# Performance work log

Hardware: AMD Instinct MI355X
Metric: run time of the kernel (lower is better)

The kernel has to match this reference:

```python
import jax, jax.numpy as jnp
import numpy as np

NH, DQK, DV = 8, 256, 64
B, TI, TO, H, W = 8, 16, 16, 32, 32


def setup_inputs() -> dict:
    key = jax.random.key(0)
    ks = jax.random.split(key, 10)
    def wn(k, shape, fan_in):
        return jax.random.normal(k, shape, jnp.float32) * (1.0 / np.sqrt(fan_in)).astype(np.float32)
    return {
        "v": jax.random.normal(ks[0], (B, TI, DV, H, W), jnp.float32),
        "k": jax.random.normal(ks[1], (B, TI, DQK), jnp.float32),
        "q": jax.random.normal(ks[2], (B, TO, DQK), jnp.float32),
        "prod_mask": jax.random.randint(ks[3], (B, TO, TI), 0, 2, jnp.int32),
        "Wq": wn(ks[4], (DQK, NH * DQK), DQK),   # q_layer: Linear(d_qk, nh*d_qk)
        "bq": jnp.zeros((NH * DQK,), jnp.float32),
        "Wk": wn(ks[5], (DQK, NH * DQK), DQK),   # k_layer
        "bk": jnp.zeros((NH * DQK,), jnp.float32),
        "Wv": wn(ks[6], (NH * DV, DV, 3, 3), DV * 9),  # v_layer: Conv2d(d_v, nh*d_v, 3, pad=1), OIHW
        "bv": jnp.zeros((NH * DV,), jnp.float32),
        "Wp": wn(ks[7], (DV, NH * DV, 1, 1), NH * DV),  # proj_concat: Conv2d(nh*d_v, d_v, 1)
        "bp": jnp.zeros((DV,), jnp.float32),
    }


def _conv(x, w, b, pad):
    y = jax.lax.conv_general_dilated(
        x, w, window_strides=(1, 1), padding=[(pad, pad), (pad, pad)],
        dimension_numbers=("NCHW", "OIHW", "NCHW"))
    return y + b[None, :, None, None]


def reference(v, k, q, prod_mask, Wq, bq, Wk, bk, Wv, bv, Wp, bp):
    Bv, Ti, dv, Hh, Ww = v.shape
    To = q.shape[1]
    # linear projections, split into heads (chunk along feature dim == contiguous blocks)
    pq = (q @ Wq + bq).reshape(Bv, To, NH, DQK)
    pk = (k @ Wk + bk).reshape(Bv, Ti, NH, DQK)
    # 3x3 conv projection of values over all B*T_i frames
    pv = _conv(v.reshape(Bv * Ti, dv, Hh, Ww), Wv, bv, 1).reshape(Bv, Ti, NH, dv, Hh, Ww)
    # scaled dot-product attention, all heads at once
    scores = jnp.einsum("bohd,bihd->bhoi", pq, pk) / jnp.sqrt(jnp.float32(DQK))
    scores = jnp.where(prod_mask[:, None, :, :] == 0, jnp.float32(-1e10), scores)
    weights = jax.nn.softmax(scores, axis=-1)  # softmax over T_i
    pv_flat = pv.reshape(Bv, Ti, NH, dv * Hh * Ww)
    att = jnp.einsum("bhoi,bihf->bohf", weights, pv_flat)  # [B,To,NH,dv*H*W]
    # concat heads along channel dim, then 1x1 conv projection
    concat = att.reshape(Bv * To, NH * dv, Hh, Ww)
    out = _conv(concat, Wp, bp, 0)
    return out.reshape(Bv, To, dv, Hh, Ww)
```

## Files before the change

kernel.cpp:

```cpp
#include <hip/hip_runtime.h>
#include <hip/hip_fp16.h>

#define NH_   8
#define DQK_  256
#define DV_   64
#define NB_   8
#define TI_   16
#define TO_   16
#define HH_   32
#define WW_   32
#define FR_   (NB_*TI_)
#define PX_   (HH_*WW_)

typedef _Float16 f16x8 __attribute__((ext_vector_type(8)));
typedef _Float16 f16x4 __attribute__((ext_vector_type(4)));
typedef float    f32x4 __attribute__((ext_vector_type(4)));

__global__ __launch_bounds__(256) void k_prep(const float* __restrict__ v,
                                              _Float16* __restrict__ v16t) {
    int blk = blockIdx.x;
    int f = blk >> 2;
    int px = ((blk & 3) << 8) + threadIdx.x;
    const float* src = v + (size_t)f * DV_ * PX_;
    _Float16* dst = v16t + (size_t)f * PX_ * DV_ + (size_t)px * DV_;
    f16x8 buf[8];
    #pragma unroll
    for (int cg = 0; cg < 8; ++cg) {
        #pragma unroll
        for (int j = 0; j < 8; ++j)
            buf[cg][j] = (_Float16)src[(cg * 8 + j) * PX_ + px];
    }
    #pragma unroll
    for (int cg = 0; cg < 8; ++cg)
        *(f16x8*)(dst + cg * 8) = buf[cg];
}

__global__ void k_proj(const float* __restrict__ q, const float* __restrict__ kk,
                       const float* __restrict__ Wq, const float* __restrict__ bq,
                       const float* __restrict__ Wk, const float* __restrict__ bk,
                       float* __restrict__ pq, float* __restrict__ pk) {
    __shared__ float qs[32][256];
    int mat = blockIdx.z;
    const float* X  = mat ? kk : q;
    const float* Wm = mat ? Wk : Wq;
    const float* bm = mat ? bk : bq;
    float* out = mat ? pk : pq;
    int t = threadIdx.x;
    int by = blockIdx.y;
    for (int idx = t; idx < 32 * 256; idx += 256) {
        int r = idx >> 8, k2 = idx & 255;
        qs[r][k2] = X[(by * 32 + r) * 256 + k2];
    }
    __syncthreads();
    int nd = blockIdx.x * 64 + (t & 63);
    int jb = (t >> 6) * 8;
    float a[8];
    #pragma unroll
    for (int j = 0; j < 8; ++j) a[j] = 0.f;
    for (int k2 = 0; k2 < 256; ++k2) {
        float wv = Wm[k2 * 2048 + nd];
        #pragma unroll
        for (int j = 0; j < 8; ++j) a[j] += qs[jb + j][k2] * wv;
    }
    float bb = bm[nd];
    #pragma unroll
    for (int j = 0; j < 8; ++j)
        out[(size_t)(by * 32 + jb + j) * 2048 + nd] = a[j] + bb;
}

__global__ void k_scores(const float* __restrict__ pq, const float* __restrict__ pk,
                         const int* __restrict__ mask, float* __restrict__ wsm) {
    __shared__ float lq[16][256];
    __shared__ float lk[16][257];
    int b = blockIdx.x >> 3, n = blockIdx.x & 7;
    int t = threadIdx.x;
    for (int idx = t; idx < 4096; idx += 256) {
        int r = idx >> 8, dd = idx & 255;
        lq[r][dd] = pq[(size_t)(b * 16 + r) * 2048 + n * 256 + dd];
        lk[r][dd] = pk[(size_t)(b * 16 + r) * 2048 + n * 256 + dd];
    }
    __syncthreads();
    int o = t >> 4, i = t & 15;
    float s = 0.f;
    for (int dd = 0; dd < 256; ++dd) s += lq[o][dd] * lk[i][dd];
    s *= 0.0625f;
    if (mask[(b * 16 + o) * 16 + i] == 0) s = -1e10f;
    float mx = s;
    #pragma unroll
    for (int off = 1; off < 16; off <<= 1) mx = fmaxf(mx, __shfl_xor(mx, off, 16));
    float e = __expf(s - mx);
    float sum = e;
    #pragma unroll
    for (int off = 1; off < 16; off <<= 1) sum += __shfl_xor(sum, off, 16);
    wsm[((size_t)(b * 8 + n) * 16 + o) * 16 + i] = e / sum;
}

__global__ void k_fold(const float* __restrict__ Wp, const float* __restrict__ Wv,
                       _Float16* __restrict__ Wf2) {
    int gid = blockIdx.x * 256 + threadIdx.x;
    int l = gid & 63;
    int oct16 = (gid >> 6) & 31;
    int cg = (gid >> 11) & 1;
    int r = gid >> 12;
    int oc = oct16 * 16 + (l & 15);
    int n = oc >> 6, d = oc & 63;
    int cbase = cg * 32 + (l >> 4) * 8;
    float acc[8];
    #pragma unroll
    for (int j = 0; j < 8; ++j) acc[j] = 0.f;
    for (int c2 = 0; c2 < 64; ++c2) {
        float wp = Wp[d * 512 + n * 64 + c2];
        #pragma unroll
        for (int j = 0; j < 8; ++j)
            acc[j] += wp * Wv[((n * 64 + c2) * 64 + cbase + j) * 9 + r];
    }
    #pragma unroll
    for (int j = 0; j < 8; ++j) Wf2[(size_t)gid * 8 + j] = (_Float16)acc[j];
}

__global__ void k_foldbias(const float* __restrict__ Wp, const float* __restrict__ bv,
                           const float* __restrict__ bp, float* __restrict__ bias_out) {
    int d = threadIdx.x;
    float acc = bp[d];
    for (int oc = 0; oc < 512; ++oc) acc += Wp[d * 512 + oc] * bv[oc];
    bias_out[d] = acc;
}

__global__ __launch_bounds__(256) void k_conv(const _Float16* __restrict__ v16t,
                                              const _Float16* __restrict__ Wf2,
                                              _Float16* __restrict__ g) {
    __shared__ _Float16 slab[204 * 64];
    int f = blockIdx.z, mblk = blockIdx.y, pxblk = blockIdx.x;
    int t = threadIdx.x;
    int l = t & 63, wm = t >> 6;

    const _Float16* vb = v16t + (size_t)f * PX_ * DV_;
    for (int task = t; task < 204 * 8; task += 256) {
        int pos = task >> 3, sl = task & 7;
        int yy = pos / 34;
        int xx = pos - yy * 34;
        int y = pxblk * 4 + yy - 1;
        int x = xx - 1;
        uint4 val = make_uint4(0u, 0u, 0u, 0u);
        if ((unsigned)y < 32u && (unsigned)x < 32u)
            val = *(const uint4*)(vb + (y * 32 + x) * 64 + sl * 8);
        int off = pos * 128 + ((sl ^ (pos & 7)) << 4);
        *(uint4*)((char*)slab + off) = val;
    }
    __syncthreads();

    int m = l & 15, kg = l >> 4;
    int pos0[8];
    #pragma unroll
    for (int nt = 0; nt < 8; ++nt) {
        int pxl = nt * 16 + m;
        pos0[nt] = (pxl >> 5) * 34 + (pxl & 31);
    }

    const f16x8* Wf8 = (const f16x8*)Wf2;
    f32x4 acc[2][8];
    #pragma unroll
    for (int mt = 0; mt < 2; ++mt)
        #pragma unroll
        for (int nt = 0; nt < 8; ++nt)
            acc[mt][nt] = (f32x4){0.f, 0.f, 0.f, 0.f};

    #pragma unroll
    for (int cg = 0; cg < 2; ++cg) {
        int slotb = (cg * 4 + kg) << 4;
        #pragma unroll
        for (int r = 0; r < 9; ++r) {
            int dd = (r / 3) * 34 + (r % 3);
            int abase = (r * 2 + cg) * 32 + mblk * 8 + wm * 2;
            f16x8 af0 = Wf8[(size_t)(abase + 0) * 64 + l];
            f16x8 af1 = Wf8[(size_t)(abase + 1) * 64 + l];
            f16x8 bf[8];
            #pragma unroll
            for (int nt = 0; nt < 8; ++nt) {
                int pos = pos0[nt] + dd;
                int off = pos * 128 + (slotb ^ ((pos & 7) << 4));
                bf[nt] = *(const f16x8*)((const char*)slab + off);
            }
            #pragma unroll
            for (int nt = 0; nt < 8; ++nt) {
                acc[0][nt] = __builtin_amdgcn_mfma_f32_16x16x32_f16(af0, bf[nt], acc[0][nt], 0, 0, 0);
                acc[1][nt] = __builtin_amdgcn_mfma_f32_16x16x32_f16(af1, bf[nt], acc[1][nt], 0, 0, 0);
            }
        }
    }

    _Float16* gb = g + (size_t)f * 512 * 1024 + (size_t)pxblk * 128;
    #pragma unroll
    for (int mt = 0; mt < 2; ++mt) {
        int ocbase = (mblk * 8 + wm * 2 + mt) * 16 + kg * 4;
        #pragma unroll
        for (int nt = 0; nt < 8; ++nt) {
            int px = nt * 16 + m;
            #pragma unroll
            for (int e = 0; e < 4; ++e)
                gb[(size_t)(ocbase + e) * 1024 + px] = (_Float16)acc[mt][nt][e];
        }
    }
}

__global__ void k_comb(const _Float16* __restrict__ g, const float* __restrict__ wsm,
                       const float* __restrict__ bias_out, float* __restrict__ out) {
    __shared__ float wl[2048];
    int d = blockIdx.y, b = blockIdx.z;
    int t = threadIdx.x;
    for (int idx = t; idx < 2048; idx += 256) wl[idx] = wsm[(size_t)b * 2048 + idx];
    __syncthreads();
    int px0 = t * 4;
    float acc[16][4];
    #pragma unroll
    for (int o = 0; o < 16; ++o)
        #pragma unroll
        for (int e = 0; e < 4; ++e) acc[o][e] = 0.f;

    for (int i = 0; i < 16; ++i) {
        #pragma unroll
        for (int n = 0; n < 8; ++n) {
            const _Float16* gp = g + ((size_t)((b * 16 + i) * 512 + n * 64 + d)) * 1024 + px0;
            f16x4 hv = *(const f16x4*)gp;
            float g0 = (float)hv[0], g1 = (float)hv[1], g2 = (float)hv[2], g3 = (float)hv[3];
            #pragma unroll
            for (int o = 0; o < 16; ++o) {
                float wv = wl[n * 256 + o * 16 + i];
                acc[o][0] += wv * g0;
                acc[o][1] += wv * g1;
                acc[o][2] += wv * g2;
                acc[o][3] += wv * g3;
            }
        }
    }
    float bo = bias_out[d];
    #pragma unroll
    for (int o = 0; o < 16; ++o) {
        float4 res = make_float4(acc[o][0] + bo, acc[o][1] + bo, acc[o][2] + bo, acc[o][3] + bo);
        *(float4*)(out + ((size_t)((b * 16 + o) * 64 + d)) * 1024 + px0) = res;
    }
}

extern "C" void kernel_launch(void* const* d_in, const int* in_sizes, int n_in,
                              void* d_out, int out_size, void* d_ws, size_t ws_size,
                              hipStream_t stream) {
    (void)in_sizes; (void)n_in; (void)out_size;
    const float* v  = (const float*)d_in[0];
    const float* kk = (const float*)d_in[1];
    const float* q  = (const float*)d_in[2];
    const int*   pm = (const int*)d_in[3];
    const float* Wq = (const float*)d_in[4];
    const float* bq = (const float*)d_in[5];
    const float* Wk = (const float*)d_in[6];
    const float* bk = (const float*)d_in[7];
    const float* Wv = (const float*)d_in[8];
    const float* bv = (const float*)d_in[9];
    const float* Wp = (const float*)d_in[10];
    const float* bp = (const float*)d_in[11];
    float* out = (float*)d_out;

    char* ws = (char*)d_ws;
    size_t o_v16t = 0;
    size_t o_g    = o_v16t + (size_t)FR_ * PX_ * DV_ * 2;
    size_t o_wf2  = o_g    + (size_t)FR_ * 512 * PX_ * 2;
    size_t o_pq   = o_wf2  + (size_t)9 * 2 * 32 * 64 * 8 * 2;
    size_t o_pk   = o_pq   + (size_t)128 * 2048 * 4;
    size_t o_wsm  = o_pk   + (size_t)128 * 2048 * 4;
    size_t o_bias = o_wsm  + (size_t)NB_ * NH_ * TO_ * TI_ * 4;
    size_t need   = o_bias + 256;
    if (ws_size < need) return;

    _Float16* v16t = (_Float16*)(ws + o_v16t);
    _Float16* g    = (_Float16*)(ws + o_g);
    _Float16* Wf2  = (_Float16*)(ws + o_wf2);
    float* pq      = (float*)(ws + o_pq);
    float* pk      = (float*)(ws + o_pk);
    float* wsm     = (float*)(ws + o_wsm);
    float* bias    = (float*)(ws + o_bias);

    k_prep<<<dim3(512), dim3(256), 0, stream>>>(v, v16t);
    k_proj<<<dim3(32, 4, 2), dim3(256), 0, stream>>>(q, kk, Wq, bq, Wk, bk, pq, pk);
    k_scores<<<dim3(64), dim3(256), 0, stream>>>(pq, pk, pm, wsm);
    k_fold<<<dim3(144), dim3(256), 0, stream>>>(Wp, Wv, Wf2);
    k_foldbias<<<dim3(1), dim3(64), 0, stream>>>(Wp, bv, bp, bias);
    k_conv<<<dim3(8, 4, FR_), dim3(256), 0, stream>>>(v16t, Wf2, g);
    k_comb<<<dim3(1, 64, NB_), dim3(256), 0, stream>>>(g, wsm, bias, out);
}
```

Before: 321.7 us.

## Enlarge conv tiles to 512-thread blocks and stage fold weights in LDS

```diff
diff --git a/kernel.cpp b/kernel.cpp
--- a/kernel.cpp
+++ b/kernel.cpp
@@ -57,6 +57,7 @@
     float a[8];
     #pragma unroll
     for (int j = 0; j < 8; ++j) a[j] = 0.f;
+    #pragma unroll 8
     for (int k2 = 0; k2 < 256; ++k2) {
         float wv = Wm[k2 * 2048 + nd];
         #pragma unroll
@@ -95,27 +96,47 @@
     wsm[((size_t)(b * 8 + n) * 16 + o) * 16 + i] = e / sum;
 }
 
-__global__ void k_fold(const float* __restrict__ Wp, const float* __restrict__ Wv,
-                       _Float16* __restrict__ Wf2) {
-    int gid = blockIdx.x * 256 + threadIdx.x;
-    int l = gid & 63;
-    int oct16 = (gid >> 6) & 31;
-    int cg = (gid >> 11) & 1;
-    int r = gid >> 12;
-    int oc = oct16 * 16 + (l & 15);
-    int n = oc >> 6, d = oc & 63;
-    int cbase = cg * 32 + (l >> 4) * 8;
-    float acc[8];
-    #pragma unroll
-    for (int j = 0; j < 8; ++j) acc[j] = 0.f;
+__global__ __launch_bounds__(256) void k_fold(const float* __restrict__ Wp,
+                                              const float* __restrict__ Wv,
+                                              _Float16* __restrict__ Wf2) {
+    __shared__ float Wvs[64][64];
+    __shared__ float Wps[64][65];
+    int n = blockIdx.x & 7, r = blockIdx.x >> 3;
+    int t = threadIdx.x;
+    #pragma unroll
+    for (int k = 0; k < 16; ++k) {
+        int idx = t + 256 * k;
+        int a2 = idx >> 6, bcol = idx & 63;
+        Wvs[a2][bcol] = Wv[(size_t)(n * 64 + a2) * 576 + bcol * 9 + r];
+        Wps[a2][bcol] = Wp[(size_t)a2 * 512 + n * 64 + bcol];
+    }
+    __syncthreads();
+    int d = t & 63, cq = t >> 6;
+    float acc[2][8];
+    #pragma unroll
+    for (int jj = 0; jj < 2; ++jj)
+        #pragma unroll
+        for (int j = 0; j < 8; ++j) acc[jj][j] = 0.f;
     for (int c2 = 0; c2 < 64; ++c2) {
-        float wp = Wp[d * 512 + n * 64 + c2];
-        #pragma unroll
-        for (int j = 0; j < 8; ++j)
-            acc[j] += wp * Wv[((n * 64 + c2) * 64 + cbase + j) * 9 + r];
-    }
-    #pragma unroll
-    for (int j = 0; j < 8; ++j) Wf2[(size_t)gid * 8 + j] = (_Float16)acc[j];
+        float wp = Wps[d][c2];
+        const float* row = &Wvs[c2][cq * 16];
+        #pragma unroll
+        for (int j = 0; j < 8; ++j) acc[0][j] += wp * row[j];
+        #pragma unroll
+        for (int j = 0; j < 8; ++j) acc[1][j] += wp * row[8 + j];
+    }
+    #pragma unroll
+    for (int jj = 0; jj < 2; ++jj) {
+        int cbase = cq * 16 + jj * 8;
+        int cg = cbase >> 5;
+        int lane = (d & 15) | (((cbase & 31) >> 3) << 4);
+        int oct16 = n * 4 + (d >> 4);
+        int gid = r * 4096 + cg * 2048 + oct16 * 64 + lane;
+        f16x8 o8;
+        #pragma unroll
+        for (int j = 0; j < 8; ++j) o8[j] = (_Float16)acc[jj][j];
+        *(f16x8*)&Wf2[(size_t)gid * 8] = o8;
+    }
 }
 
 __global__ void k_foldbias(const float* __restrict__ Wp, const float* __restrict__ bv,
@@ -126,20 +147,22 @@
     bias_out[d] = acc;
 }
 
-__global__ __launch_bounds__(256) void k_conv(const _Float16* __restrict__ v16t,
-                                              const _Float16* __restrict__ Wf2,
-                                              _Float16* __restrict__ g) {
-    __shared__ _Float16 slab[204 * 64];
-    int f = blockIdx.z, mblk = blockIdx.y, pxblk = blockIdx.x;
-    int t = threadIdx.x;
-    int l = t & 63, wm = t >> 6;
+__global__ __launch_bounds__(512, 2) void k_conv(const _Float16* __restrict__ v16t,
+                                                 const _Float16* __restrict__ Wf2,
+                                                 _Float16* __restrict__ g) {
+    __shared__ _Float16 slab[340 * 64];
+    int f = blockIdx.z, ocb = blockIdx.y, pxb = blockIdx.x;
+    int t = threadIdx.x;
+    int l = t & 63, wv = t >> 6;
+    int wmM = wv >> 2, wmN = wv & 3;
 
     const _Float16* vb = v16t + (size_t)f * PX_ * DV_;
-    for (int task = t; task < 204 * 8; task += 256) {
+    int y0 = pxb * 8;
+    for (int task = t; task < 340 * 8; task += 512) {
         int pos = task >> 3, sl = task & 7;
         int yy = pos / 34;
         int xx = pos - yy * 34;
-        int y = pxblk * 4 + yy - 1;
+        int y = y0 + yy - 1;
         int x = xx - 1;
         uint4 val = make_uint4(0u, 0u, 0u, 0u);
         if ((unsigned)y < 32u && (unsigned)x < 32u)
@@ -150,55 +173,58 @@
     __syncthreads();
 
     int m = l & 15, kg = l >> 4;
-    int pos0[8];
-    #pragma unroll
-    for (int nt = 0; nt < 8; ++nt) {
-        int pxl = nt * 16 + m;
+    int pos0[4];
+    #pragma unroll
+    for (int nt = 0; nt < 4; ++nt) {
+        int pxl = wmN * 64 + nt * 16 + m;
         pos0[nt] = (pxl >> 5) * 34 + (pxl & 31);
     }
 
     const f16x8* Wf8 = (const f16x8*)Wf2;
-    f32x4 acc[2][8];
-    #pragma unroll
-    for (int mt = 0; mt < 2; ++mt)
-        #pragma unroll
-        for (int nt = 0; nt < 8; ++nt)
+    f32x4 acc[8][4];
+    #pragma unroll
+    for (int mt = 0; mt < 8; ++mt)
+        #pragma unroll
+        for (int nt = 0; nt < 4; ++nt)
             acc[mt][nt] = (f32x4){0.f, 0.f, 0.f, 0.f};
 
     #pragma unroll
-    for (int cg = 0; cg < 2; ++cg) {
+    for (int s = 0; s < 18; ++s) {
+        int cg = s / 9, r = s - 9 * (s / 9);
+        int dd = (r / 3) * 34 + (r % 3);
         int slotb = (cg * 4 + kg) << 4;
-        #pragma unroll
-        for (int r = 0; r < 9; ++r) {
-            int dd = (r / 3) * 34 + (r % 3);
-            int abase = (r * 2 + cg) * 32 + mblk * 8 + wm * 2;
-            f16x8 af0 = Wf8[(size_t)(abase + 0) * 64 + l];
-            f16x8 af1 = Wf8[(size_t)(abase + 1) * 64 + l];
-            f16x8 bf[8];
+        int abase = (r * 2 + cg) * 32 + ocb * 16 + wmM * 8;
+
+        f16x8 afv[8];
+        #pragma unroll
+        for (int mt = 0; mt < 8; ++mt)
+            afv[mt] = Wf8[(size_t)(abase + mt) * 64 + l];
+
+        f16x8 bfv[4];
+        #pragma unroll
+        for (int nt = 0; nt < 4; ++nt) {
+            int pos = pos0[nt] + dd;
+            int off = pos * 128 + (slotb ^ ((pos & 7) << 4));
+            bfv[nt] = *(const f16x8*)((const char*)slab + off);
+        }
+
+        #pragma unroll
+        for (int mt = 0; mt < 8; ++mt)
             #pragma unroll
-            for (int nt = 0; nt < 8; ++nt) {
-                int pos = pos0[nt] + dd;
-                int off = pos * 128 + (slotb ^ ((pos & 7) << 4));
-                bf[nt] = *(const f16x8*)((const char*)slab + off);
-            }
-            #pragma unroll
-            for (int nt = 0; nt < 8; ++nt) {
-                acc[0][nt] = __builtin_amdgcn_mfma_f32_16x16x32_f16(af0, bf[nt], acc[0][nt], 0, 0, 0);
-                acc[1][nt] = __builtin_amdgcn_mfma_f32_16x16x32_f16(af1, bf[nt], acc[1][nt], 0, 0, 0);
-            }
-        }
-    }
-
-    _Float16* gb = g + (size_t)f * 512 * 1024 + (size_t)pxblk * 128;
-    #pragma unroll
-    for (int mt = 0; mt < 2; ++mt) {
-        int ocbase = (mblk * 8 + wm * 2 + mt) * 16 + kg * 4;
-        #pragma unroll
-        for (int nt = 0; nt < 8; ++nt) {
-            int px = nt * 16 + m;
+            for (int nt = 0; nt < 4; ++nt)
+                acc[mt][nt] = __builtin_amdgcn_mfma_f32_16x16x32_f16(afv[mt], bfv[nt], acc[mt][nt], 0, 0, 0);
+    }
+
+    _Float16* gb = g + (size_t)f * 512 * 1024;
+    #pragma unroll
+    for (int mt = 0; mt < 8; ++mt) {
+        int oc0 = (ocb * 16 + wmM * 8 + mt) * 16 + kg * 4;
+        #pragma unroll
+        for (int nt = 0; nt < 4; ++nt) {
+            int px = pxb * 256 + wmN * 64 + nt * 16 + m;
             #pragma unroll
             for (int e = 0; e < 4; ++e)
-                gb[(size_t)(ocbase + e) * 1024 + px] = (_Float16)acc[mt][nt][e];
+                gb[(size_t)(oc0 + e) * 1024 + px] = (_Float16)acc[mt][nt][e];
         }
     }
 }
@@ -217,6 +243,7 @@
         #pragma unroll
         for (int e = 0; e < 4; ++e) acc[o][e] = 0.f;
 
+    #pragma unroll 2
     for (int i = 0; i < 16; ++i) {
         #pragma unroll
         for (int n = 0; n < 8; ++n) {
@@ -281,8 +308,8 @@
     k_prep<<<dim3(512), dim3(256), 0, stream>>>(v, v16t);
     k_proj<<<dim3(32, 4, 2), dim3(256), 0, stream>>>(q, kk, Wq, bq, Wk, bk, pq, pk);
     k_scores<<<dim3(64), dim3(256), 0, stream>>>(pq, pk, pm, wsm);
-    k_fold<<<dim3(144), dim3(256), 0, stream>>>(Wp, Wv, Wf2);
+    k_fold<<<dim3(72), dim3(256), 0, stream>>>(Wp, Wv, Wf2);
     k_foldbias<<<dim3(1), dim3(64), 0, stream>>>(Wp, bv, bp, bias);
-    k_conv<<<dim3(8, 4, FR_), dim3(256), 0, stream>>>(v16t, Wf2, g);
+    k_conv<<<dim3(4, 2, FR_), dim3(512), 0, stream>>>(v16t, Wf2, g);
     k_comb<<<dim3(1, 64, NB_), dim3(256), 0, stream>>>(g, wsm, bias, out);
 }
```

Result: slower. 809.4 us (+151.6%).
